# Optimization experiments

Hardware: AMD Instinct MI355X
Metric: run time of the kernel (lower is better)

Reference implementation:

```python
import jax, jax.numpy as jnp
import numpy as np

H, W = 80, 80
LOWPASS = 0.3   # 3DGS low-pass filter added to 2D covariance diagonal
NEAR = 0.2      # near-plane cull depth


def quat_to_rot(q):
    # q: [N,4] (w,x,y,z) -> [N,3,3]
    w, x, y, z = q[..., 0], q[..., 1], q[..., 2], q[..., 3]
    return jnp.stack([
        jnp.stack([1 - 2 * (y * y + z * z), 2 * (x * y - w * z), 2 * (x * z + w * y)], -1),
        jnp.stack([2 * (x * y + w * z), 1 - 2 * (x * x + z * z), 2 * (y * z - w * x)], -1),
        jnp.stack([2 * (x * z - w * y), 2 * (y * z + w * x), 1 - 2 * (x * x + y * y)], -1),
    ], -2)


def setup_inputs() -> dict:
    key = jax.random.key(0)
    k1, k2 = jax.random.split(key)
    vsize = 1.25
    def mids(lo, hi, lim):
        g = np.arange(lo, hi + 1e-6, vsize)
        return ((g[:-1] + g[1:]) / 2.0)[:lim]
    xy = mids(-20.0, 20.0, 200)   # 32 midpoints
    zz = mids(-4.0, 4.0, 16)      # 6 midpoints
    X, Y, Z = np.meshgrid(xy, xy, zz, indexing='ij')
    pc_xyz = jnp.asarray(np.stack([X, Y, Z], -1).reshape(-1, 3), jnp.float32)  # [6144,3]
    N = pc_xyz.shape[0]
    B, NC, C = 1, 6, 32
    vox_features = jax.random.normal(k1, (B, N, C), jnp.float32)
    density = jax.random.normal(k2, (B, N), jnp.float32)
    scales = jnp.full((N, 1), float(np.log(vsize)), jnp.float32)
    rots = jnp.concatenate([jnp.ones((N, 1)), jnp.zeros((N, 3))], -1).astype(jnp.float32)
    # 6 surround cameras at origin, yaw = k*60deg; cam axes: x=right, y=up-ish, z=forward
    yaws = np.arange(NC) * (2 * np.pi / NC)
    f = np.stack([np.cos(yaws), np.sin(yaws), np.zeros(NC)], -1)
    r = np.stack([np.sin(yaws), -np.cos(yaws), np.zeros(NC)], -1)
    u = np.cross(f, r)
    Rw2c = np.stack([r, u, f], 1)  # rows are camera axes -> world2cam rotation [NC,3,3]
    cam_rot = jnp.asarray(Rw2c[None], jnp.float32)          # [B,NC,3,3]
    cam_trans = jnp.zeros((B, NC, 3), jnp.float32)          # [B,NC,3]
    cam_intr = jnp.asarray(np.tile(np.array([45.0, 45.0, W / 2.0, H / 2.0], np.float32), (B, NC, 1)))
    return dict(vox_features=vox_features, density=density, cam_rot=cam_rot,
                cam_trans=cam_trans, cam_intr=cam_intr, pc_xyz=pc_xyz,
                scales=scales, rots=rots)


def _render_one(Rcw, t, intr, pc_xyz, Mcov, opacity, feats):
    # Rcw [3,3], t [3], intr [4]; Mcov [N,3,3] = R*diag(s); opacity [N]; feats [N,C]
    fx, fy, cx, cy = intr[0], intr[1], intr[2], intr[3]
    cam = pc_xyz @ Rcw.T + t                    # [N,3] camera-frame means
    tz = jnp.maximum(cam[:, 2], 1e-6)
    valid = (cam[:, 2] > NEAR).astype(pc_xyz.dtype)
    u = fx * cam[:, 0] / tz + cx
    v = fy * cam[:, 1] / tz + cy
    z0 = jnp.zeros_like(tz)
    J = jnp.stack([jnp.stack([fx / tz, z0, -fx * cam[:, 0] / tz ** 2], -1),
                   jnp.stack([z0, fy / tz, -fy * cam[:, 1] / tz ** 2], -1)], -2)  # [N,2,3]
    A = jnp.einsum('nij,jk->nik', J, Rcw)       # J @ W  [N,2,3]
    Bm = jnp.einsum('nij,njk->nik', A, Mcov)    # [N,2,3]
    cov = jnp.einsum('nij,nkj->nik', Bm, Bm)    # 2D covariance [N,2,2]
    a = cov[:, 0, 0] + LOWPASS
    b = cov[:, 0, 1]
    c = cov[:, 1, 1] + LOWPASS
    det = a * c - b * b
    ia, ib, ic = c / det, -b / det, a / det
    # depth-sort (invalid gaussians pushed to the back)
    order = jnp.argsort(tz + (1.0 - valid) * 1e6)
    u, v, ia, ib, ic = u[order], v[order], ia[order], ib[order], ic[order]
    op_s, feat_s, valid_s = opacity[order], feats[order], valid[order]
    px = jnp.arange(W, dtype=pc_xyz.dtype)
    py = jnp.arange(H, dtype=pc_xyz.dtype)
    dx = px[None, None, :] - u[:, None, None]   # [N,1,W] -> broadcast [N,H,W]
    dy = py[None, :, None] - v[:, None, None]   # [N,H,1]
    power = (-0.5 * (ia[:, None, None] * dx * dx + ic[:, None, None] * dy * dy)
             - ib[:, None, None] * dx * dy)
    g = jnp.exp(jnp.minimum(power, 0.0))
    alpha = jnp.clip(op_s[:, None, None] * g, 0.0, 0.99) * valid_s[:, None, None]
    Tcum = jnp.cumprod(1.0 - alpha, axis=0)
    Texc = jnp.concatenate([jnp.ones((1, H, W), alpha.dtype), Tcum[:-1]], 0)  # exclusive transmittance
    return jnp.einsum('nhw,nc->chw', Texc * alpha, feat_s)


def reference(vox_features, density, cam_rot, cam_trans, cam_intr, pc_xyz, scales, rots):
    Bsz, N, C = vox_features.shape
    Rg = quat_to_rot(rots)                      # [N,3,3]
    s = jnp.exp(scales)                         # [N,1] isotropic scale
    Mcov = Rg * s[:, :, None]                   # R @ diag(s,s,s)
    outs = []
    for b in range(Bsz):
        op = jax.nn.softplus(density[b]).reshape(-1)        # opacity activation
        feats = vox_features[b].reshape(-1, C)
        def rone(args):
            R_, t_, K_ = args
            return _render_one(R_, t_, K_, pc_xyz, Mcov, op, feats)
        out_b = jax.lax.map(rone, (cam_rot[b], cam_trans[b], cam_intr[b]))  # [NC,C,H,W]
        outs.append(out_b)
    return jnp.stack(outs)                      # [B,NC,C,H,W]
```

## Files before the change

### kernel.cpp

```cpp
#include <hip/hip_runtime.h>

#define NEARV    0.2f
#define LOWPASSV 0.3f

constexpr int HH = 80, WW = 80;
constexpr int CFE = 32;
constexpr int NZ = 6;

constexpr int NCELL = 1024;
constexpr int HMAX = NCELL * NZ;

typedef unsigned long long u64;
typedef unsigned int u32;

__global__ __launch_bounds__(512) void rank_kernel(
    const float* __restrict__ pc_xyz, const float* __restrict__ cam_rot,
    const float* __restrict__ cam_trans, int N,
    int* __restrict__ counts, int* __restrict__ cellord)
{
  __shared__ u32 sk[NCELL];
  __shared__ u32 wred[8];

  const int cam = blockIdx.y;
  const int tid = threadIdx.x;
  const float* R = cam_rot + cam*9;
  const float R20 = R[6], R21 = R[7], R22 = R[8];
  const float t2  = cam_trans[cam*3+2];

  int vcnt = 0;
  #pragma unroll
  for (int e2 = 0; e2 < NCELL/512; ++e2) {
    const int cell = e2*512 + tid;
    const int i0 = cell * NZ;
    u32 key22 = 0x3FFFFFu;
    if (i0 < N) {
      float c2 = R20*pc_xyz[i0*3+0] + R21*pc_xyz[i0*3+1] + R22*pc_xyz[i0*3+2] + t2;
      if (c2 > NEARV) {
        u32 b = __float_as_uint(c2) - 0x3E000000u;
        b = b < 0x03FFFF00u ? b : 0x03FFFF00u;
        key22 = b >> 4;
        ++vcnt;
      }
    }
    sk[cell] = (key22 << 10) | (u32)cell;
  }
  __syncthreads();

  const int cell = blockIdx.x * 256 + (tid >> 1);
  const u32 mykey = sk[cell];
  const uint4* k4 = (const uint4*)sk;
  const int h0 = (tid & 1) * (NCELL/8);
  int rank = 0;
  #pragma unroll 8
  for (int i = 0; i < NCELL/8; ++i) {
    const uint4 kv = k4[h0 + i];
    rank += (int)(kv.x < mykey) + (int)(kv.y < mykey)
          + (int)(kv.z < mykey) + (int)(kv.w < mykey);
  }
  rank += __shfl_xor(rank, 1, 64);

  if ((tid & 1) == 0)
    cellord[(size_t)cam * NCELL + rank] = cell;

  if (blockIdx.x == 0) {
    #pragma unroll
    for (int off = 32; off > 0; off >>= 1) vcnt += __shfl_down(vcnt, off, 64);
    if ((tid & 63) == 0) wred[tid >> 6] = (u32)vcnt;
    __syncthreads();
    if (tid == 0) {
      u32 tot = 0;
      #pragma unroll
      for (int w = 0; w < 8; ++w) tot += wred[w];
      counts[cam] = (int)tot * NZ;
    }
  }
}

__global__ __launch_bounds__(256) void proj_kernel(
    const float* __restrict__ pc_xyz, const float* __restrict__ cam_rot,
    const float* __restrict__ cam_trans, const float* __restrict__ cam_intr,
    const float* __restrict__ density, const float* __restrict__ scales,
    int N, int NC,
    const int* __restrict__ counts, const int* __restrict__ cellord,
    float4* __restrict__ hdrA, float4* __restrict__ hdrB)
{
  const int cam = blockIdx.y;
  const int kq = blockIdx.x * 256 + threadIdx.x;
  if (kq >= counts[cam]) return;

  const int cellp = kq / NZ;
  const int n = cellord[(size_t)cam * NCELL + cellp] * NZ + (kq - cellp * NZ);

  const float* R = cam_rot + cam*9;
  const float* t = cam_trans + cam*3;
  const float* intr = cam_intr + cam*4;
  const float fx = intr[0], fy = intr[1], cx = intr[2], cy = intr[3];
  const int b = cam / NC;

  const float p0 = pc_xyz[n*3+0], p1 = pc_xyz[n*3+1], p2 = pc_xyz[n*3+2];
  const float c0 = R[0]*p0 + R[1]*p1 + R[2]*p2 + t[0];
  const float c1 = R[3]*p0 + R[4]*p1 + R[5]*p2 + t[1];
  const float c2 = R[6]*p0 + R[7]*p1 + R[8]*p2 + t[2];
  const float tz = fmaxf(c2, 1e-6f);
  const float itz = 1.0f / tz;
  const float u = fx*c0*itz + cx;
  const float v = fy*c1*itz + cy;
  const float j00 = fx*itz, j02 = -(fx*c0*itz)*itz;
  const float j11 = fy*itz, j12 = -(fy*c1*itz)*itz;
  const float s = expf(scales[n]);
  const float s2 = s*s;
  const float cov00 = s2*(j00*j00 + j02*j02);
  const float cov01 = s2*(j02*j12);
  const float cov11 = s2*(j11*j11 + j12*j12);
  const float a = cov00 + LOWPASSV, bb = cov01, cc = cov11 + LOWPASSV;
  const float det = a*cc - bb*bb;
  const float idet = 1.0f / det;
  const float mid = 0.5f*(a + cc);
  const float dd = sqrtf(fmaxf(mid*mid - det, 0.f));
  float r2 = 32.f * (mid + dd);
  const float dens = density[(size_t)b*N + n];
  const float op = fmaxf(dens, 0.f) + log1pf(expf(-fabsf(dens)));
  const float sx = fminf(fmaxf(u, 0.f), (float)(WW-1)) - u;
  const float sy = fminf(fmaxf(v, 0.f), (float)(HH-1)) - v;
  if (sx*sx + sy*sy > r2) r2 = -1.0f;

  const float L = 1.4426950408889634f;
  const float A2 = -0.5f * (cc*idet) * L;
  const float C2 = -0.5f * (a*idet)  * L;
  const float B2 =         (bb*idet) * L;

  hdrA[(size_t)cam * HMAX + kq] = make_float4(u, v, A2, B2);
  hdrB[(size_t)cam * HMAX + kq] = make_float4(C2, op, r2, __int_as_float(n));
}

__global__ __launch_bounds__(64) void render_kernel(
    const float* __restrict__ vox,
    const float4* __restrict__ hdrA, const float4* __restrict__ hdrB,
    const int* __restrict__ counts,
    float* __restrict__ out, int N, int NC)
{
  __shared__ int   cgi[64];
  __shared__ float4 sfeat[64];

  const int cam = blockIdx.y;
  const int tile = blockIdx.x;
  const int tx = tile % (WW/16), ty = tile / (WW/16);
  const int lane = threadIdx.x;
  const int lx = lane & 15, ly = lane >> 4;
  const int px = tx*16 + lx, py = ty*4 + ly;
  const float fpx = (float)px, fpy = (float)py;
  const float tx0 = (float)(tx*16), tx1 = tx0 + 15.f;
  const float ty0 = (float)(ty*4),  ty1 = ty0 + 3.f;
  const int count = counts[cam];
  const int b = cam / NC;
  const float4* hA = hdrA + (size_t)cam * HMAX;
  const float4* hB = hdrB + (size_t)cam * HMAX;
  const float4* voxb = (const float4*)vox + (size_t)b * N * (CFE/4);

  float acc[CFE];
  #pragma unroll
  for (int i = 0; i < CFE; ++i) acc[i] = 0.f;
  float T = 1.0f;
  bool done = false;

#define RDLN(x, l) __uint_as_float(__builtin_amdgcn_readlane(__float_as_uint(x), (l)))

#define LOAD4(Aarr, Barr, base_) do {                                   \
    _Pragma("unroll")                                                   \
    for (int d_ = 0; d_ < 4; ++d_) {                                    \
      const int kn_ = min((base_) + d_*64 + lane, count - 1);           \
      Aarr[d_] = hA[kn_]; Barr[d_] = hB[kn_];                           \
    } } while (0)

#define PROCESS_CHUNK(k0_, a0_, b0_) do {                               \
    const int ki = (k0_) + lane;                                        \
       \
    const float gu = (a0_).x, gv = (a0_).y;                             \
    const float gA = (a0_).z, gB = (a0_).w, gC = (b0_).x;               \
    const float dxl = tx0 - gu, dxh = tx1 - gu;                         \
    const float dyl = ty0 - gv, dyh = ty1 - gv;                         \
    const float X = fmaxf(dxl, fminf(0.f, dxh));                        \
    const float Y = fmaxf(dyl, fminf(0.f, dyh));                        \
    const float dyv = fmaxf(dyl, fminf((gB*X) / (-2.0f*gC), dyh));      \
    const float P1 = gA*X*X + gC*dyv*dyv + gB*X*dyv;                    \
    const float dxv = fmaxf(dxl, fminf((gB*Y) / (-2.0f*gA), dxh));      \
    const float P2 = gA*dxv*dxv + gC*Y*Y + gB*dxv*Y;                    \
    const bool hit = (ki < count) && (fmaxf(P1, P2) > -23.0831f);       \
    const u64 m = __ballot(hit);                                        \
    const int P = __popcll(m);                                          \
    if (P == 0) continue;                                               \
    if (hit) {                                                          \
      const int pos = (int)__popcll(m & ((1ull << lane) - 1ull));       \
      cgi[pos] = __float_as_int((b0_).w);                               \
    }                                                                   \
    __builtin_amdgcn_wave_barrier();   \
    const int sl = lane >> 3, sc = lane & 7;                            \
    float4 pf = voxb[(size_t)cgi[min(sl, P - 1)] * (CFE/4) + sc];       \
    u64 mm_ = m;                       \
    for (int j = 0; j < P; j += 8) {                                    \
            \
      float al[8];                                                      \
      _Pragma("unroll")                                                 \
      for (int qq = 0; qq < 8; ++qq) {                                  \
        const int idx = j + qq;                                         \
        int lq = 0;                                                     \
        if (mm_) { lq = (int)__builtin_ctzll(mm_); mm_ &= mm_ - 1; }    \
        const float su  = RDLN((a0_).x, lq);                            \
        const float sv  = RDLN((a0_).y, lq);                            \
        const float sA2 = RDLN((a0_).z, lq);                            \
        const float sB2 = RDLN((a0_).w, lq);                            \
        const float sC2 = RDLN((b0_).x, lq);                            \
        const float sop = RDLN((b0_).y, lq);                            \
        const float dx = fpx - su, dy = fpy - sv;                       \
        const float pl2 = sA2*(dx*dx) + sC2*(dy*dy) + sB2*(dx*dy);      \
        float av = fminf(sop * __builtin_exp2f(fminf(pl2, 0.f)), 0.99f); \
        av = (pl2 > -23.0831f) ? av : 0.f;       \
        al[qq] = (idx < P) ? av : 0.f;                                  \
      }                                                                 \
      sfeat[lane] = pf;                            \
      if (j + 8 < P) {                            \
        const int si = min(j + 8 + sl, P - 1);                          \
        pf = voxb[(size_t)cgi[si] * (CFE/4) + sc];                      \
      }                                                                 \
      __builtin_amdgcn_wave_barrier();   \
      _Pragma("unroll")                                                 \
      for (int qq = 0; qq < 8; ++qq) {                                  \
        const float w = T * al[qq];                                     \
        T -= w;                                                         \
        if (__any(w > 1e-8f)) {                                         \
          const float4* fj = &sfeat[qq * 8];                            \
          _Pragma("unroll")                                             \
          for (int c8 = 0; c8 < CFE/4; ++c8) {                          \
            const float4 fv = fj[c8];                                   \
            acc[c8*4+0] = fmaf(w, fv.x, acc[c8*4+0]);                   \
            acc[c8*4+1] = fmaf(w, fv.y, acc[c8*4+1]);                   \
            acc[c8*4+2] = fmaf(w, fv.z, acc[c8*4+2]);                   \
            acc[c8*4+3] = fmaf(w, fv.w, acc[c8*4+3]);                   \
          }                                                             \
        }                                                               \
      }                                                                 \
      if (__all(T < 1e-3f)) { done = true; break; }                     \
      __builtin_amdgcn_wave_barrier();  \
    }                                                                   \
  } while (0)

  if (count > 0) {
    float4 A0x[4], B0x[4], A1x[4], B1x[4];
    const int nquad = (count + 255) >> 8;
    LOAD4(A0x, B0x, 0);

    for (int q = 0; q < nquad && !done; q += 2) {
      if (q + 1 < nquad) LOAD4(A1x, B1x, (q+1)*256);
      #pragma unroll
      for (int d = 0; d < 4; ++d) {
        if (done) break;
        const int k0 = q*256 + d*64;
        if (k0 >= count) break;
        PROCESS_CHUNK(k0, A0x[d], B0x[d]);
      }
      if (done || q + 1 >= nquad) break;
      if (q + 2 < nquad) LOAD4(A0x, B0x, (q+2)*256);
      #pragma unroll
      for (int d = 0; d < 4; ++d) {
        if (done) break;
        const int k0 = (q+1)*256 + d*64;
        if (k0 >= count) break;
        PROCESS_CHUNK(k0, A1x[d], B1x[d]);
      }
    }
  }
#undef PROCESS_CHUNK
#undef LOAD4
#undef RDLN

  float* ob = out + (((size_t)cam * CFE) * HH + py) * WW + px;
  #pragma unroll
  for (int c = 0; c < CFE; ++c) ob[(size_t)c * HH * WW] = acc[c];
}

extern "C" void kernel_launch(void* const* d_in, const int* in_sizes, int n_in,
                              void* d_out, int out_size, void* d_ws, size_t ws_size,
                              hipStream_t stream) {
  const float* vox       = (const float*)d_in[0];
  const float* density   = (const float*)d_in[1];
  const float* cam_rot   = (const float*)d_in[2];
  const float* cam_trans = (const float*)d_in[3];
  const float* cam_intr  = (const float*)d_in[4];
  const float* pc_xyz    = (const float*)d_in[5];
  const float* scales    = (const float*)d_in[6];
  float* out = (float*)d_out;

  const int N    = in_sizes[5] / 3;
  const int NCAM = in_sizes[4] / 4;
  const int B    = in_sizes[1] / N;
  const int NC   = NCAM / B;

  unsigned char* ws = (unsigned char*)d_ws;
  int* countsPtr = (int*)ws;
  int* cellord   = (int*)(ws + 256);
  float4* hdrA   = (float4*)(ws + 32768);
  float4* hdrB   = (float4*)(ws + 32768 + (size_t)NCAM * HMAX * sizeof(float4));

  rank_kernel<<<dim3(NCELL/256, NCAM), 512, 0, stream>>>(
      pc_xyz, cam_rot, cam_trans, N, countsPtr, cellord);
  proj_kernel<<<dim3((HMAX + 255) / 256, NCAM), 256, 0, stream>>>(
      pc_xyz, cam_rot, cam_trans, cam_intr, density, scales, N, NC,
      countsPtr, cellord, hdrA, hdrB);
  render_kernel<<<dim3((WW/16)*(HH/4), NCAM), 64, 0, stream>>>(
      vox, hdrA, hdrB, countsPtr, out, N, NC);
}
```

Measured before the change: 83.25 us.

## Fuse depth ranking and Gaussian projection into a single prep kernel

Merges the rank kernel and the projection kernel. Each block ranks 64 cells against all cell depth keys in shared memory, then projects those cells' Gaussians and scatters the headers directly to their sorted positions. This removes one kernel launch and the global cellord intermediate. In exchange, every block recomputes the full key array, and culled Gaussians are also projected and written beyond the valid count.

Measured after the change: 80.69 us. 3.1% less time.

```diff
diff --git a/kernel.cpp b/kernel.cpp
--- a/kernel.cpp
+++ b/kernel.cpp
@@ -13,24 +13,29 @@
 typedef unsigned long long u64;
 typedef unsigned int u32;
 
-__global__ __launch_bounds__(512) void rank_kernel(
+__global__ __launch_bounds__(256) void prep_kernel(
     const float* __restrict__ pc_xyz, const float* __restrict__ cam_rot,
-    const float* __restrict__ cam_trans, int N,
-    int* __restrict__ counts, int* __restrict__ cellord)
+    const float* __restrict__ cam_trans, const float* __restrict__ cam_intr,
+    const float* __restrict__ density, const float* __restrict__ scales,
+    int N, int NC,
+    int* __restrict__ counts, float4* __restrict__ hdrA,
+    float4* __restrict__ hdrB)
 {
   __shared__ u32 sk[NCELL];
-  __shared__ u32 wred[8];
+  __shared__ int rnk[64];
+  __shared__ u32 wred[4];
 
   const int cam = blockIdx.y;
   const int tid = threadIdx.x;
   const float* R = cam_rot + cam*9;
+  const float* t = cam_trans + cam*3;
   const float R20 = R[6], R21 = R[7], R22 = R[8];
-  const float t2  = cam_trans[cam*3+2];
+  const float t2  = t[2];
 
   int vcnt = 0;
   #pragma unroll
-  for (int e2 = 0; e2 < NCELL/512; ++e2) {
-    const int cell = e2*512 + tid;
+  for (int e4 = 0; e4 < NCELL/256; ++e4) {
+    const int cell = e4*256 + tid;
     const int i0 = cell * NZ;
     u32 key22 = 0x3FFFFFu;
     if (i0 < N) {
@@ -46,91 +51,80 @@
   }
   __syncthreads();
 
-  const int cell = blockIdx.x * 256 + (tid >> 1);
-  const u32 mykey = sk[cell];
+  const int cbase = blockIdx.x * 64;
+  const int cl = tid >> 2;
+  const int q  = tid & 3;
+  const u32 mykey = sk[cbase + cl];
   const uint4* k4 = (const uint4*)sk;
-  const int h0 = (tid & 1) * (NCELL/8);
-  int rank = 0;
+  int r = 0;
   #pragma unroll 8
-  for (int i = 0; i < NCELL/8; ++i) {
-    const uint4 kv = k4[h0 + i];
-    rank += (int)(kv.x < mykey) + (int)(kv.y < mykey)
-          + (int)(kv.z < mykey) + (int)(kv.w < mykey);
-  }
-  rank += __shfl_xor(rank, 1, 64);
-
-  if ((tid & 1) == 0)
-    cellord[(size_t)cam * NCELL + rank] = cell;
+  for (int i = 0; i < 64; ++i) {
+    const uint4 kv = k4[q*64 + i];
+    r += (int)(kv.x < mykey) + (int)(kv.y < mykey)
+       + (int)(kv.z < mykey) + (int)(kv.w < mykey);
+  }
+  r += __shfl_xor(r, 1, 64);
+  r += __shfl_xor(r, 2, 64);
+  if (q == 0) rnk[cl] = r;
 
   if (blockIdx.x == 0) {
     #pragma unroll
     for (int off = 32; off > 0; off >>= 1) vcnt += __shfl_down(vcnt, off, 64);
     if ((tid & 63) == 0) wred[tid >> 6] = (u32)vcnt;
-    __syncthreads();
-    if (tid == 0) {
-      u32 tot = 0;
-      #pragma unroll
-      for (int w = 0; w < 8; ++w) tot += wred[w];
-      counts[cam] = (int)tot * NZ;
-    }
-  }
-}
-
-__global__ __launch_bounds__(256) void proj_kernel(
-    const float* __restrict__ pc_xyz, const float* __restrict__ cam_rot,
-    const float* __restrict__ cam_trans, const float* __restrict__ cam_intr,
-    const float* __restrict__ density, const float* __restrict__ scales,
-    int N, int NC,
-    const int* __restrict__ counts, const int* __restrict__ cellord,
-    float4* __restrict__ hdrA, float4* __restrict__ hdrB)
-{
-  const int cam = blockIdx.y;
-  const int kq = blockIdx.x * 256 + threadIdx.x;
-  if (kq >= counts[cam]) return;
-
-  const int cellp = kq / NZ;
-  const int n = cellord[(size_t)cam * NCELL + cellp] * NZ + (kq - cellp * NZ);
-
-  const float* R = cam_rot + cam*9;
-  const float* t = cam_trans + cam*3;
+  }
+  __syncthreads();
+  if (blockIdx.x == 0 && tid == 0)
+    counts[cam] = (int)(wred[0] + wred[1] + wred[2] + wred[3]) * NZ;
+
   const float* intr = cam_intr + cam*4;
   const float fx = intr[0], fy = intr[1], cx = intr[2], cy = intr[3];
+  const float R0=R[0],R1=R[1],R2=R[2],R3=R[3],R4=R[4],R5=R[5];
+  const float t0=t[0],t1=t[1];
   const int b = cam / NC;
-
-  const float p0 = pc_xyz[n*3+0], p1 = pc_xyz[n*3+1], p2 = pc_xyz[n*3+2];
-  const float c0 = R[0]*p0 + R[1]*p1 + R[2]*p2 + t[0];
-  const float c1 = R[3]*p0 + R[4]*p1 + R[5]*p2 + t[1];
-  const float c2 = R[6]*p0 + R[7]*p1 + R[8]*p2 + t[2];
-  const float tz = fmaxf(c2, 1e-6f);
-  const float itz = 1.0f / tz;
-  const float u = fx*c0*itz + cx;
-  const float v = fy*c1*itz + cy;
-  const float j00 = fx*itz, j02 = -(fx*c0*itz)*itz;
-  const float j11 = fy*itz, j12 = -(fy*c1*itz)*itz;
-  const float s = expf(scales[n]);
-  const float s2 = s*s;
-  const float cov00 = s2*(j00*j00 + j02*j02);
-  const float cov01 = s2*(j02*j12);
-  const float cov11 = s2*(j11*j11 + j12*j12);
-  const float a = cov00 + LOWPASSV, bb = cov01, cc = cov11 + LOWPASSV;
-  const float det = a*cc - bb*bb;
-  const float idet = 1.0f / det;
-  const float mid = 0.5f*(a + cc);
-  const float dd = sqrtf(fmaxf(mid*mid - det, 0.f));
-  float r2 = 32.f * (mid + dd);
-  const float dens = density[(size_t)b*N + n];
-  const float op = fmaxf(dens, 0.f) + log1pf(expf(-fabsf(dens)));
-  const float sx = fminf(fmaxf(u, 0.f), (float)(WW-1)) - u;
-  const float sy = fminf(fmaxf(v, 0.f), (float)(HH-1)) - v;
-  if (sx*sx + sy*sy > r2) r2 = -1.0f;
-
-  const float L = 1.4426950408889634f;
-  const float A2 = -0.5f * (cc*idet) * L;
-  const float C2 = -0.5f * (a*idet)  * L;
-  const float B2 =         (bb*idet) * L;
-
-  hdrA[(size_t)cam * HMAX + kq] = make_float4(u, v, A2, B2);
-  hdrB[(size_t)cam * HMAX + kq] = make_float4(C2, op, r2, __int_as_float(n));
+  float4* hA = hdrA + (size_t)cam * HMAX;
+  float4* hB = hdrB + (size_t)cam * HMAX;
+
+  for (int g = tid; g < 64*NZ; g += 256) {
+    const int cl2 = g / NZ, iz = g - cl2*NZ;
+    const int n  = (cbase + cl2) * NZ + iz;
+    const int kq = rnk[cl2] * NZ + iz;
+    if (n >= N) continue;
+
+    const float p0 = pc_xyz[n*3+0], p1 = pc_xyz[n*3+1], p2 = pc_xyz[n*3+2];
+    const float c0 = R0*p0 + R1*p1 + R2*p2 + t0;
+    const float c1 = R3*p0 + R4*p1 + R5*p2 + t1;
+    const float c2 = R20*p0 + R21*p1 + R22*p2 + t2;
+    const float tz = fmaxf(c2, 1e-6f);
+    const float itz = 1.0f / tz;
+    const float u = fx*c0*itz + cx;
+    const float v = fy*c1*itz + cy;
+    const float j00 = fx*itz, j02 = -(fx*c0*itz)*itz;
+    const float j11 = fy*itz, j12 = -(fy*c1*itz)*itz;
+    const float s = expf(scales[n]);
+    const float s2 = s*s;
+    const float cov00 = s2*(j00*j00 + j02*j02);
+    const float cov01 = s2*(j02*j12);
+    const float cov11 = s2*(j11*j11 + j12*j12);
+    const float a = cov00 + LOWPASSV, bb = cov01, cc = cov11 + LOWPASSV;
+    const float det = a*cc - bb*bb;
+    const float idet = 1.0f / det;
+    const float mid = 0.5f*(a + cc);
+    const float dd = sqrtf(fmaxf(mid*mid - det, 0.f));
+    float r2 = 32.f * (mid + dd);
+    const float dens = density[(size_t)b*N + n];
+    const float op = fmaxf(dens, 0.f) + log1pf(expf(-fabsf(dens)));
+    const float sx = fminf(fmaxf(u, 0.f), (float)(WW-1)) - u;
+    const float sy = fminf(fmaxf(v, 0.f), (float)(HH-1)) - v;
+    if (sx*sx + sy*sy > r2) r2 = -1.0f;
+
+    const float L = 1.4426950408889634f;
+    const float A2 = -0.5f * (cc*idet) * L;
+    const float C2 = -0.5f * (a*idet)  * L;
+    const float B2 =         (bb*idet) * L;
+
+    hA[kq] = make_float4(u, v, A2, B2);
+    hB[kq] = make_float4(C2, op, r2, __int_as_float(n));
+  }
 }
 
 __global__ __launch_bounds__(64) void render_kernel(
@@ -198,7 +192,6 @@
     float4 pf = voxb[(size_t)cgi[min(sl, P - 1)] * (CFE/4) + sc];       \
     u64 mm_ = m;                       \
     for (int j = 0; j < P; j += 8) {                                    \
-            \
       float al[8];                                                      \
       _Pragma("unroll")                                                 \
       for (int qq = 0; qq < 8; ++qq) {                                  \
@@ -297,15 +290,12 @@
 
   unsigned char* ws = (unsigned char*)d_ws;
   int* countsPtr = (int*)ws;
-  int* cellord   = (int*)(ws + 256);
   float4* hdrA   = (float4*)(ws + 32768);
   float4* hdrB   = (float4*)(ws + 32768 + (size_t)NCAM * HMAX * sizeof(float4));
 
-  rank_kernel<<<dim3(NCELL/256, NCAM), 512, 0, stream>>>(
-      pc_xyz, cam_rot, cam_trans, N, countsPtr, cellord);
-  proj_kernel<<<dim3((HMAX + 255) / 256, NCAM), 256, 0, stream>>>(
+  prep_kernel<<<dim3(NCELL/64, NCAM), 256, 0, stream>>>(
       pc_xyz, cam_rot, cam_trans, cam_intr, density, scales, N, NC,
-      countsPtr, cellord, hdrA, hdrB);
+      countsPtr, hdrA, hdrB);
   render_kernel<<<dim3((WW/16)*(HH/4), NCAM), 64, 0, stream>>>(
       vox, hdrA, hdrB, countsPtr, out, N, NC);
 }
```
